# Optimization experiments

Hardware: AMD Instinct MI355X
Metric: run time of the kernel (lower is better)

The kernel has to match this reference:

```python
import jax, jax.numpy as jnp
import numpy as np

N_HEAD = 16
DIMS = 1024

def setup_inputs() -> dict:
    key = jax.random.key(0)
    ks = jax.random.split(key, 5)
    B, T, C = 4, 2048, DIMS
    std = 1.0 / np.sqrt(C)
    x = jax.random.normal(ks[0], (B, T, C), dtype=jnp.float32)
    W_attn = jax.random.normal(ks[1], (C, 3 * C), dtype=jnp.float32) * std
    b_attn = jnp.zeros((3 * C,), dtype=jnp.float32)
    W_proj = jax.random.normal(ks[2], (C, C), dtype=jnp.float32) * std
    b_proj = jnp.zeros((C,), dtype=jnp.float32)
    return {"x": x, "W_attn": W_attn, "b_attn": b_attn, "W_proj": W_proj, "b_proj": b_proj}

def reference(x, W_attn, b_attn, W_proj, b_proj):
    B, T, C = x.shape
    H = N_HEAD
    D = C // H
    qkv = x @ W_attn + b_attn  # [B,T,3C]
    q, k, v = jnp.split(qkv, 3, axis=-1)
    # [B,T,C] -> [B,H,T,D]
    q = q.reshape(B, T, H, D).transpose(0, 2, 1, 3)
    k = k.reshape(B, T, H, D).transpose(0, 2, 1, 3)
    v = v.reshape(B, T, H, D).transpose(0, 2, 1, 3)
    att = jnp.einsum('bhqd,bhkd->bhqk', q, k) * (1.0 / np.sqrt(D))
    causal = jnp.tril(jnp.ones((T, T), dtype=bool))  # [T,T]
    att = jnp.where(causal[None, None, :, :], att, -jnp.inf)
    att = jax.nn.softmax(att, axis=-1)
    # dropout p=0.0 -> identity in eval/zero-prob mode
    y = jnp.einsum('bhqk,bhkd->bhqd', att, v)  # [B,H,T,D]
    y = y.transpose(0, 2, 1, 3).reshape(B, T, C)
    y = y @ W_proj + b_proj
    return y
```

## Files before the change

### kernel.cpp

```cpp
#include <hip/hip_runtime.h>
#include <hip/hip_bf16.h>
#include <stdint.h>

typedef unsigned short u16;
typedef unsigned int   u32;

using short8 = __attribute__((ext_vector_type(8))) short;
using f32x4  = __attribute__((ext_vector_type(4))) float;

__device__ __forceinline__ float b2f(u32 u) {
    union { u32 i; float f; } v;
    v.i = u << 16;
    return v.f;
}
__device__ __forceinline__ u16 f2b(float f) {
    union { float f; u32 i; } v; v.f = f;
    u32 x = v.i;
    x += 0x7fffu + ((x >> 16) & 1u);
    return (u16)(x >> 16);
}
__device__ __forceinline__ u32 pkbf16(float lo, float hi) {
    __hip_bfloat162 h = __float22bfloat162_rn(float2{lo, hi});
    return *reinterpret_cast<u32*>(&h);
}
__device__ __forceinline__ float fexp2(float x) {
#if __has_builtin(__builtin_amdgcn_exp2f)
    return __builtin_amdgcn_exp2f(x);
#else
    return exp2f(x);
#endif
}
__device__ __forceinline__ u32 perm_lo(u32 a, u32 b) {
#if __has_builtin(__builtin_amdgcn_perm)
    return __builtin_amdgcn_perm(b, a, 0x05040100u);
#else
    return (a & 0xffffu) | (b << 16);
#endif
}
__device__ __forceinline__ u32 perm_hi(u32 a, u32 b) {
#if __has_builtin(__builtin_amdgcn_perm)
    return __builtin_amdgcn_perm(b, a, 0x07060302u);
#else
    return (a >> 16) | (b & 0xffff0000u);
#endif
}

__device__ __forceinline__ void gll16(const u16* g, u16* l) {
    __builtin_amdgcn_global_load_lds(
        (const __attribute__((address_space(1))) void*)g,
        (__attribute__((address_space(3))) void*)l, 16, 0, 0);
}

__global__ __launch_bounds__(256)
void cast_bf16(const float* __restrict__ in, u16* __restrict__ out, int n)
{
    const int i = (blockIdx.x * 256 + threadIdx.x) * 8;
    if (i >= n) return;
    const float4 a = *reinterpret_cast<const float4*>(in + i);
    const float4 b = *reinterpret_cast<const float4*>(in + i + 4);
    *reinterpret_cast<uint4*>(out + i) = make_uint4(
        pkbf16(a.x, a.y), pkbf16(a.z, a.w), pkbf16(b.x, b.y), pkbf16(b.z, b.w));
}

__global__ __launch_bounds__(256)
void transpose_cast(const float* __restrict__ W, u16* __restrict__ Wt, int R, int Ncols)
{
    __shared__ float t[32][33];
    const int c0 = blockIdx.x * 32, r0 = blockIdx.y * 32;
    const int lx = threadIdx.x & 31, ly = threadIdx.x >> 5;
#pragma unroll
    for (int i = 0; i < 4; i++) {
        const int r = ly + i * 8;
        t[r][lx] = W[(size_t)(r0 + r) * Ncols + c0 + lx];
    }
    __syncthreads();
#pragma unroll
    for (int i = 0; i < 4; i++) {
        const int c = ly + i * 8;
        Wt[(size_t)(c0 + c) * R + r0 + lx] = f2b(t[lx][c]);
    }
}

template<typename OT>
__global__ __launch_bounds__(256)
void gemm_mfma(const u16* __restrict__ A, const u16* __restrict__ Bt,
               const float* __restrict__ bias, OT* __restrict__ C,
               int M, int N, int K)
{
    __shared__ u16 As[128 * 32];
    __shared__ u16 Bs[128 * 32];

    const int tid  = threadIdx.x;
    const int w    = tid >> 6;
    const int lane = tid & 63;
    const int quad = lane >> 4;
    const int c16  = lane & 15;
    const int wr   = w >> 1, wc = w & 1;

    const int m0 = blockIdx.y * 128;
    const int n0 = blockIdx.x * 128;

    const int srow = w * 32 + (lane >> 2);
    const int skc  = (lane & 3) * 8;
    const u16* gA = A  + (size_t)(m0 + srow) * K + skc;
    const u16* gB = Bt + (size_t)(n0 + srow) * K + skc;
    u16* lA = As + w * 32 * 32 + lane * 8;
    u16* lB = Bs + w * 32 * 32 + lane * 8;

    f32x4 acc[4][4];
#pragma unroll
    for (int i = 0; i < 4; i++)
#pragma unroll
        for (int j = 0; j < 4; j++) acc[i][j] = (f32x4){0.f, 0.f, 0.f, 0.f};

    for (int k0 = 0; k0 < K; k0 += 32) {
        __syncthreads();
        gll16(gA + k0,                  lA);
        gll16(gA + k0 + 16 * (size_t)K, lA + 16 * 32);
        gll16(gB + k0,                  lB);
        gll16(gB + k0 + 16 * (size_t)K, lB + 16 * 32);
        __syncthreads();

        short8 af[4], bf[4];
#pragma unroll
        for (int i = 0; i < 4; i++)
            af[i] = *reinterpret_cast<const short8*>(&As[(wr * 64 + i * 16 + c16) * 32 + quad * 8]);
#pragma unroll
        for (int j = 0; j < 4; j++)
            bf[j] = *reinterpret_cast<const short8*>(&Bs[(wc * 64 + j * 16 + c16) * 32 + quad * 8]);
#pragma unroll
        for (int i = 0; i < 4; i++)
#pragma unroll
            for (int j = 0; j < 4; j++)
                acc[i][j] = __builtin_amdgcn_mfma_f32_16x16x32_bf16(af[i], bf[j], acc[i][j], 0, 0, 0);
    }

#pragma unroll
    for (int i = 0; i < 4; i++)
#pragma unroll
        for (int j = 0; j < 4; j++) {
            const int colg = n0 + wc * 64 + j * 16 + c16;
            const float bv = bias[colg];
#pragma unroll
            for (int r = 0; r < 4; r++) {
                const int rowg = m0 + wr * 64 + i * 16 + quad * 4 + r;
                const float v = acc[i][j][r] + bv;
                if constexpr (sizeof(OT) == 2)
                    ((u16*)C)[(size_t)rowg * N + colg] = f2b(v);
                else
                    ((float*)C)[(size_t)rowg * N + colg] = v;
            }
        }
}

__global__ __launch_bounds__(512, 2)
void gemm_mfma_256(const u16* __restrict__ A, const u16* __restrict__ Bt,
                   const float* __restrict__ bias, u16* __restrict__ C,
                   int M, int N, int K)
{
    __shared__ u16 ring[4 * 16384];

    const int tid  = threadIdx.x;
    const int w    = tid >> 6;
    const int lane = tid & 63;
    const int quad = lane >> 4;
    const int c16  = lane & 15;
    const int wr   = w >> 2;
    const int wc   = w & 3;

    const int nwg  = gridDim.x * gridDim.y;
    const int orig = blockIdx.y * gridDim.x + blockIdx.x;
    const int swz  = (orig & 7) * (nwg >> 3) + (orig >> 3);
    const int bx   = swz % gridDim.x;
    const int by   = swz / gridDim.x;
    const int m0   = by * 256, n0 = bx * 256;

    const int r0s = w * 16 + (lane >> 2);
    const int qs  = (lane & 3) ^ ((r0s >> 1) & 3);
    const u16* gA = A  + (size_t)(m0 + r0s) * K + qs * 8;
    const u16* gB = Bt + (size_t)(n0 + r0s) * K + qs * 8;
    const size_t hstep = (size_t)128 * K;
    u16* dstB = ring + w * 512 + lane * 8;

    const int slot = quad ^ ((c16 >> 1) & 3);
    const int aoff = (wr * 128 + c16) * 32 + slot * 8;
    const int boff = 8192 + (wc * 64 + c16) * 32 + slot * 8;

    f32x4 acc[8][4];
#pragma unroll
    for (int i = 0; i < 8; i++)
#pragma unroll
        for (int j = 0; j < 4; j++) acc[i][j] = (f32x4){0.f, 0.f, 0.f, 0.f};

    const int nt = K >> 5;

#pragma unroll
    for (int t = 0; t < 3; t++) {
        u16* db = dstB + t * 16384;
        const size_t ko = (size_t)t * 32;
        gll16(gA + ko,         db);
        gll16(gA + ko + hstep, db + 4096);
        gll16(gB + ko,         db + 8192);
        gll16(gB + ko + hstep, db + 12288);
    }

#pragma unroll 1
    for (int t = 0; t < nt; t++) {
        const int remain = nt - 1 - t;
        if (remain >= 2)      asm volatile("s_waitcnt vmcnt(8)" ::: "memory");
        else if (remain == 1) asm volatile("s_waitcnt vmcnt(4)" ::: "memory");
        else                  asm volatile("s_waitcnt vmcnt(0)" ::: "memory");
        asm volatile("s_barrier" ::: "memory");

        const u16* buf = ring + (t & 3) * 16384;
        const bool pf  = (t + 3) < nt;
        u16* db = dstB + ((t + 3) & 3) * 16384;
        const size_t ko = (size_t)(t + 3) * 32;

        short8 bfr[4], afr[4];

#pragma unroll
        for (int j = 0; j < 4; j++)
            bfr[j] = *reinterpret_cast<const short8*>(buf + boff + j * 512);
#pragma unroll
        for (int i = 0; i < 4; i++)
            afr[i] = *reinterpret_cast<const short8*>(buf + aoff + i * 512);
        if (pf) { gll16(gA + ko, db); gll16(gA + ko + hstep, db + 4096); }
        asm volatile("s_waitcnt lgkmcnt(0)" ::: "memory");
        __builtin_amdgcn_sched_barrier(0);
        __builtin_amdgcn_s_setprio(1);
#pragma unroll
        for (int i = 0; i < 4; i++)
#pragma unroll
            for (int j = 0; j < 4; j++)
                acc[i][j] = __builtin_amdgcn_mfma_f32_16x16x32_bf16(afr[i], bfr[j], acc[i][j], 0, 0, 0);
        __builtin_amdgcn_s_setprio(0);
        asm volatile("s_barrier" ::: "memory");

#pragma unroll
        for (int i = 0; i < 4; i++)
            afr[i] = *reinterpret_cast<const short8*>(buf + aoff + (i + 4) * 512);
        if (pf) { gll16(gB + ko, db + 8192); gll16(gB + ko + hstep, db + 12288); }
        asm volatile("s_waitcnt lgkmcnt(0)" ::: "memory");
        __builtin_amdgcn_sched_barrier(0);
        __builtin_amdgcn_s_setprio(1);
#pragma unroll
        for (int i = 0; i < 4; i++)
#pragma unroll
            for (int j = 0; j < 4; j++)
                acc[i + 4][j] = __builtin_amdgcn_mfma_f32_16x16x32_bf16(afr[i], bfr[j], acc[i + 4][j], 0, 0, 0);
        __builtin_amdgcn_s_setprio(0);
        asm volatile("s_barrier" ::: "memory");
    }

    float bv[4];
#pragma unroll
    for (int j = 0; j < 4; j++) bv[j] = bias[n0 + wc * 64 + j * 16 + c16];

    const int erow = wr * 16 + quad * 4;
    const int ecol = wc * 64 + c16;
#pragma unroll
    for (int i = 0; i < 8; i++) {
#pragma unroll
        for (int j = 0; j < 4; j++)
#pragma unroll
            for (int r = 0; r < 4; r++)
                ring[(erow + r) * 264 + ecol + j * 16] = f2b(acc[i][j][r] + bv[j]);
        __syncthreads();
#pragma unroll
        for (int rr = 0; rr < 2; rr++) {
            const int lr = rr * 16 + (tid >> 5);
            const int cc = (tid & 31) * 8;
            const uint4 vvec = *reinterpret_cast<const uint4*>(&ring[lr * 264 + cc]);
            const int gr = m0 + (lr >> 4) * 128 + i * 16 + (lr & 15);
            *reinterpret_cast<uint4*>(&C[(size_t)gr * N + n0 + cc]) = vvec;
        }
        __syncthreads();
    }
}

constexpr int ALDP = 72;

struct TileState {
    f32x4 O[4];
    float m, l;
    short8 qf[2];
    int qglob;
};

__device__ __forceinline__ void tile_pass(
    const u16 (*__restrict__ Ks)[ALDP], const u16 (*__restrict__ Vt)[ALDP],
    u16* __restrict__ plrow,
    TileState& ts, int kt0, bool diag, int quad, int c16)
{
    f32x4 s[4];
    __builtin_amdgcn_s_setprio(1);
#pragma unroll
    for (int sub = 0; sub < 4; sub++) {
        short8 kf0 = *reinterpret_cast<const short8*>(&Ks[sub * 16 + c16][0 * 32 + quad * 8]);
        short8 kf1 = *reinterpret_cast<const short8*>(&Ks[sub * 16 + c16][1 * 32 + quad * 8]);
        f32x4 acc = (f32x4){0.f, 0.f, 0.f, 0.f};
        acc = __builtin_amdgcn_mfma_f32_16x16x32_bf16(kf0, ts.qf[0], acc, 0, 0, 0);
        acc = __builtin_amdgcn_mfma_f32_16x16x32_bf16(kf1, ts.qf[1], acc, 0, 0, 0);
        s[sub] = acc;
    }
    __builtin_amdgcn_s_setprio(0);

    if (diag) {
#pragma unroll
        for (int sub = 0; sub < 4; sub++)
#pragma unroll
            for (int r = 0; r < 4; r++)
                if (kt0 + sub * 16 + quad * 4 + r > ts.qglob) s[sub][r] = -INFINITY;
    }

    float m0a = fmaxf(fmaxf(s[0][0], s[0][1]), fmaxf(s[0][2], s[0][3]));
    float m1a = fmaxf(fmaxf(s[1][0], s[1][1]), fmaxf(s[1][2], s[1][3]));
    float m2a = fmaxf(fmaxf(s[2][0], s[2][1]), fmaxf(s[2][2], s[2][3]));
    float m3a = fmaxf(fmaxf(s[3][0], s[3][1]), fmaxf(s[3][2], s[3][3]));
    float mloc = fmaxf(fmaxf(m0a, m1a), fmaxf(m2a, m3a));
    mloc = fmaxf(mloc, __shfl_xor(mloc, 16));
    mloc = fmaxf(mloc, __shfl_xor(mloc, 32));

    if (!__all(mloc <= ts.m + 8.f)) {
        const float mnew = fmaxf(ts.m, mloc);
        const float al   = fexp2(ts.m - mnew);
        ts.m = mnew;
        ts.l *= al;
#pragma unroll
        for (int r = 0; r < 4; r++) {
            const float alr = __shfl(al, quad * 4 + r);
#pragma unroll
            for (int d = 0; d < 4; d++) ts.O[d][r] *= alr;
        }
    }

    float ls = 0.f;
#pragma unroll
    for (int sub = 0; sub < 4; sub++) {
#pragma unroll
        for (int r = 0; r < 4; r++) s[sub][r] = fexp2(s[sub][r] - ts.m);
        ls += (s[sub][0] + s[sub][1]) + (s[sub][2] + s[sub][3]);
        *reinterpret_cast<uint2*>(plrow + c16 * ALDP + sub * 16 + quad * 4) =
            make_uint2(pkbf16(s[sub][0], s[sub][1]), pkbf16(s[sub][2], s[sub][3]));
    }
    ls += __shfl_xor(ls, 16);
    ls += __shfl_xor(ls, 32);
    ts.l += ls;

    short8 pf[2];
#pragma unroll
    for (int c = 0; c < 2; c++)
        pf[c] = *reinterpret_cast<const short8*>(plrow + c16 * ALDP + c * 32 + quad * 8);

    __builtin_amdgcn_s_setprio(1);
#pragma unroll
    for (int dsub = 0; dsub < 4; dsub++) {
#pragma unroll
        for (int c = 0; c < 2; c++) {
            short8 vf = *reinterpret_cast<const short8*>(&Vt[dsub * 16 + c16][c * 32 + quad * 8]);
            ts.O[dsub] = __builtin_amdgcn_mfma_f32_16x16x32_bf16(pf[c], vf, ts.O[dsub], 0, 0, 0);
        }
    }
    __builtin_amdgcn_s_setprio(0);
}

__global__ __launch_bounds__(256)
void attn_flash(const u16* __restrict__ qkv, u16* __restrict__ out)
{
    constexpr int T = 2048, C = 1024, C3 = 3072;

    __shared__ u16 Ks[64][ALDP];
    __shared__ u16 Vt[64][ALDP];
    __shared__ u16 Pl[4][16][ALDP];

    const int tid  = threadIdx.x;
    const int w    = tid >> 6;
    const int lane = tid & 63;
    const int quad = lane >> 4;
    const int c16  = lane & 15;

    const int qtA = blockIdx.x;
    const int qtB = 31 - qtA;
    const int bh  = blockIdx.y;
    const int h   = bh & 15;
    const int b   = bh >> 4;

    const int kr  = tid >> 2, kc = (tid & 3) * 16;
    const int vkp = tid & 31, vdg = (tid >> 5) * 8;
    const u16* baseK = qkv + (size_t)(b * T + kr) * C3 + C + h * 64 + kc;
    const u16* baseV = qkv + (size_t)(b * T + 2 * vkp) * C3 + 2 * C + h * 64 + vdg;

    u16* plrow = &Pl[w][0][0];

    uint4 ka, kb, va, vb;

#pragma unroll 1
    for (int phase = 0; phase < 2; ++phase) {
        const int qt = phase ? qtA : qtB;

        TileState ts;
        ts.qglob = qt * 64 + w * 16 + c16;
        ts.m = -INFINITY;
        ts.l = 0.f;
#pragma unroll
        for (int d = 0; d < 4; d++) ts.O[d] = (f32x4){0.f, 0.f, 0.f, 0.f};
        constexpr float QSCALE = 0.125f * 1.44269504089f;
#pragma unroll
        for (int c = 0; c < 2; c++) {
            short8 rq = *reinterpret_cast<const short8*>(
                qkv + (size_t)(b * T + ts.qglob) * C3 + h * 64 + c * 32 + quad * 8);
#pragma unroll
            for (int j = 0; j < 8; j++)
                ts.qf[c][j] = (short)f2b(b2f((u16)rq[j]) * QSCALE);
        }

        {
            const uint4* gp = reinterpret_cast<const uint4*>(baseK);
            ka = gp[0]; kb = gp[1];
            va = *reinterpret_cast<const uint4*>(baseV);
            vb = *reinterpret_cast<const uint4*>(baseV + C3);
        }

        for (int kt = 0; kt <= qt; kt++) {
            const int kt0 = kt * 64;
            __syncthreads();
            *reinterpret_cast<uint4*>(&Ks[kr][kc])     = ka;
            *reinterpret_cast<uint4*>(&Ks[kr][kc + 8]) = kb;
            {
                const u32* aw = reinterpret_cast<const u32*>(&va);
                const u32* bw = reinterpret_cast<const u32*>(&vb);
#pragma unroll
                for (int i = 0; i < 4; i++) {
                    *reinterpret_cast<u32*>(&Vt[vdg + 2 * i][2 * vkp])     = perm_lo(aw[i], bw[i]);
                    *reinterpret_cast<u32*>(&Vt[vdg + 2 * i + 1][2 * vkp]) = perm_hi(aw[i], bw[i]);
                }
            }
            __syncthreads();

            if (kt < qt) {
                const int nk0 = (kt + 1) * 64;
                const uint4* gp = reinterpret_cast<const uint4*>(baseK + (size_t)nk0 * C3);
                ka = gp[0]; kb = gp[1];
                const u16* g0 = baseV + (size_t)nk0 * C3;
                va = *reinterpret_cast<const uint4*>(g0);
                vb = *reinterpret_cast<const uint4*>(g0 + C3);
            }

            tile_pass(Ks, Vt, plrow, ts, kt0, kt == qt, quad, c16);
        }

        const float inv = 1.0f / ts.l;
#pragma unroll
        for (int r = 0; r < 4; r++) {
            const float invr = __shfl(inv, quad * 4 + r);
            const int qrow = qt * 64 + w * 16 + quad * 4 + r;
#pragma unroll
            for (int dsub = 0; dsub < 4; dsub++)
                out[(size_t)(b * T + qrow) * C + h * 64 + dsub * 16 + c16] =
                    f2b(ts.O[dsub][r] * invr);
        }
    }
}

extern "C" void kernel_launch(void* const* d_in, const int* in_sizes, int n_in,
                              void* d_out, int out_size, void* d_ws, size_t ws_size,
                              hipStream_t stream)
{
    constexpr int B = 4, T = 2048, C = 1024;
    constexpr int M = B * T;
    const float* x      = (const float*)d_in[0];
    const float* W_attn = (const float*)d_in[1];
    const float* b_attn = (const float*)d_in[2];
    const float* W_proj = (const float*)d_in[3];
    const float* b_proj = (const float*)d_in[4];
    float* out = (float*)d_out;

    char* p = (char*)d_ws;
    u16* qkv     = (u16*)p;                 p += (size_t)M * 3 * C * sizeof(u16);
    u16* xb      = (u16*)p;
    u16* attn_o  = (u16*)p;                 p += (size_t)M * C * sizeof(u16);
    u16* Wt_attn = (u16*)p;                 p += (size_t)3 * C * C * sizeof(u16);
    u16* Wt_proj = (u16*)p;

    cast_bf16<<<dim3(M * C / (256 * 8)), 256, 0, stream>>>(x, xb, M * C);
    transpose_cast<<<dim3(3 * C / 32, C / 32), 256, 0, stream>>>(W_attn, Wt_attn, C, 3 * C);
    transpose_cast<<<dim3(C / 32, C / 32), 256, 0, stream>>>(W_proj, Wt_proj, C, C);

    gemm_mfma_256<<<dim3(3 * C / 256, M / 256), 512, 0, stream>>>(
        xb, Wt_attn, b_attn, qkv, M, 3 * C, C);

    attn_flash<<<dim3(16, B * 16), 256, 0, stream>>>(qkv, attn_o);

    gemm_mfma<float><<<dim3(C / 128, M / 128), 256, 0, stream>>>(
        attn_o, Wt_proj, b_proj, out, M, C, C);
}
```

Before: 278.2 us.

## Double-buffer K/V LDS tiles, remap blocks per XCD, defer row-sum reduction

The attention kernel now keeps two LDS buffers for K and V^T. The next tile is written after the current tile_pass, so each KV iteration needs one barrier instead of two. The row-sum cross-lane shuffle reduction moves out of the inner loop and runs once before normalization. Blocks are remapped so all query tiles of a given batch-head land on the same XCD, which should improve L2 reuse of K/V. The two weight transpose-cast launches are also merged into one. The cost is extra LDS per block, which may lower occupancy.

```diff
diff --git a/kernel.cpp b/kernel.cpp
--- a/kernel.cpp
+++ b/kernel.cpp
@@ -63,10 +63,17 @@
 }
 
 __global__ __launch_bounds__(256)
-void transpose_cast(const float* __restrict__ W, u16* __restrict__ Wt, int R, int Ncols)
+void transpose_cast2(const float* __restrict__ Wa, u16* __restrict__ Wta,
+                     const float* __restrict__ Wp, u16* __restrict__ Wtp)
 {
     __shared__ float t[32][33];
-    const int c0 = blockIdx.x * 32, r0 = blockIdx.y * 32;
+    constexpr int R = 1024;
+    const bool pa = blockIdx.x < 96;
+    const float* W  = pa ? Wa  : Wp;
+    u16*         Wt = pa ? Wta : Wtp;
+    const int Ncols = pa ? 3072 : 1024;
+    const int c0 = (pa ? blockIdx.x : blockIdx.x - 96) * 32;
+    const int r0 = blockIdx.y * 32;
     const int lx = threadIdx.x & 31, ly = threadIdx.x >> 5;
 #pragma unroll
     for (int i = 0; i < 4; i++) {
@@ -344,8 +351,6 @@
         *reinterpret_cast<uint2*>(plrow + c16 * ALDP + sub * 16 + quad * 4) =
             make_uint2(pkbf16(s[sub][0], s[sub][1]), pkbf16(s[sub][2], s[sub][3]));
     }
-    ls += __shfl_xor(ls, 16);
-    ls += __shfl_xor(ls, 32);
     ts.l += ls;
 
     short8 pf[2];
@@ -370,8 +375,8 @@
 {
     constexpr int T = 2048, C = 1024, C3 = 3072;
 
-    __shared__ u16 Ks[64][ALDP];
-    __shared__ u16 Vt[64][ALDP];
+    __shared__ u16 Ks[2][64][ALDP];
+    __shared__ u16 Vt[2][64][ALDP];
     __shared__ u16 Pl[4][16][ALDP];
 
     const int tid  = threadIdx.x;
@@ -380,11 +385,15 @@
     const int quad = lane >> 4;
     const int c16  = lane & 15;
 
-    const int qtA = blockIdx.x;
-    const int qtB = 31 - qtA;
-    const int bh  = blockIdx.y;
-    const int h   = bh & 15;
-    const int b   = bh >> 4;
+    const int flat = blockIdx.y * gridDim.x + blockIdx.x;
+    const int xcd  = flat & 7;
+    const int tt   = flat >> 3;
+    const int qp   = tt & 15;
+    const int bh   = ((tt >> 4) << 3) | xcd;
+    const int qtA  = qp;
+    const int qtB  = 31 - qp;
+    const int h    = bh & 15;
+    const int b    = bh >> 4;
 
     const int kr  = tid >> 2, kc = (tid & 3) * 16;
     const int vkp = tid & 31, vdg = (tid >> 5) * 8;
@@ -421,21 +430,21 @@
             va = *reinterpret_cast<const uint4*>(baseV);
             vb = *reinterpret_cast<const uint4*>(baseV + C3);
         }
+        __syncthreads();
+        {
+            *reinterpret_cast<uint4*>(&Ks[0][kr][kc])     = ka;
+            *reinterpret_cast<uint4*>(&Ks[0][kr][kc + 8]) = kb;
+            const u32* aw = reinterpret_cast<const u32*>(&va);
+            const u32* bw = reinterpret_cast<const u32*>(&vb);
+#pragma unroll
+            for (int i = 0; i < 4; i++) {
+                *reinterpret_cast<u32*>(&Vt[0][vdg + 2 * i][2 * vkp])     = perm_lo(aw[i], bw[i]);
+                *reinterpret_cast<u32*>(&Vt[0][vdg + 2 * i + 1][2 * vkp]) = perm_hi(aw[i], bw[i]);
+            }
+        }
 
         for (int kt = 0; kt <= qt; kt++) {
-            const int kt0 = kt * 64;
-            __syncthreads();
-            *reinterpret_cast<uint4*>(&Ks[kr][kc])     = ka;
-            *reinterpret_cast<uint4*>(&Ks[kr][kc + 8]) = kb;
-            {
-                const u32* aw = reinterpret_cast<const u32*>(&va);
-                const u32* bw = reinterpret_cast<const u32*>(&vb);
-#pragma unroll
-                for (int i = 0; i < 4; i++) {
-                    *reinterpret_cast<u32*>(&Vt[vdg + 2 * i][2 * vkp])     = perm_lo(aw[i], bw[i]);
-                    *reinterpret_cast<u32*>(&Vt[vdg + 2 * i + 1][2 * vkp]) = perm_hi(aw[i], bw[i]);
-                }
-            }
+            const int cur = kt & 1;
             __syncthreads();
 
             if (kt < qt) {
@@ -447,10 +456,26 @@
                 vb = *reinterpret_cast<const uint4*>(g0 + C3);
             }
 
-            tile_pass(Ks, Vt, plrow, ts, kt0, kt == qt, quad, c16);
-        }
-
-        const float inv = 1.0f / ts.l;
+            tile_pass(Ks[cur], Vt[cur], plrow, ts, kt * 64, kt == qt, quad, c16);
+
+            if (kt < qt) {
+                const int nxt = cur ^ 1;
+                *reinterpret_cast<uint4*>(&Ks[nxt][kr][kc])     = ka;
+                *reinterpret_cast<uint4*>(&Ks[nxt][kr][kc + 8]) = kb;
+                const u32* aw = reinterpret_cast<const u32*>(&va);
+                const u32* bw = reinterpret_cast<const u32*>(&vb);
+#pragma unroll
+                for (int i = 0; i < 4; i++) {
+                    *reinterpret_cast<u32*>(&Vt[nxt][vdg + 2 * i][2 * vkp])     = perm_lo(aw[i], bw[i]);
+                    *reinterpret_cast<u32*>(&Vt[nxt][vdg + 2 * i + 1][2 * vkp]) = perm_hi(aw[i], bw[i]);
+                }
+            }
+        }
+
+        float ls = ts.l;
+        ls += __shfl_xor(ls, 16);
+        ls += __shfl_xor(ls, 32);
+        const float inv = 1.0f / ls;
 #pragma unroll
         for (int r = 0; r < 4; r++) {
             const float invr = __shfl(inv, quad * 4 + r);
@@ -484,8 +509,7 @@
     u16* Wt_proj = (u16*)p;
 
     cast_bf16<<<dim3(M * C / (256 * 8)), 256, 0, stream>>>(x, xb, M * C);
-    transpose_cast<<<dim3(3 * C / 32, C / 32), 256, 0, stream>>>(W_attn, Wt_attn, C, 3 * C);
-    transpose_cast<<<dim3(C / 32, C / 32), 256, 0, stream>>>(W_proj, Wt_proj, C, C);
+    transpose_cast2<<<dim3(128, 32), 256, 0, stream>>>(W_attn, Wt_attn, W_proj, Wt_proj);
 
     gemm_mfma_256<<<dim3(3 * C / 256, M / 256), 512, 0, stream>>>(
         xb, Wt_attn, b_attn, qkv, M, 3 * C, C);
```

Result: slower. 284.6 us (+2.3%).
